# Optimization experiments

Measured on AMD Instinct MI355X. Metric: run time of the kernel, lower is better.

Reference implementation:

```python
import jax, jax.numpy as jnp
import numpy as np

B, T, D, H = 64, 512, 256, 512  # batch, seq_len, embed_dim, enc_units


def _lstm(x_tbd, U, xW, reverse):
    """Keras LSTM with activation='sigmoid' (all gates AND candidate/output use sigmoid).
    x_tbd: [T,B,D] (only for shape), xW: precomputed x@W+b [T,B,4H], U: [H,4H].
    Gate order in Keras kernels: i, f, c(g), o."""
    if reverse:
        xW = xW[::-1]
    b = xW.shape[1]
    h0 = jnp.zeros((b, U.shape[0]), xW.dtype)
    c0 = jnp.zeros((b, U.shape[0]), xW.dtype)

    def step(carry, xw):
        h, c = carry
        z = xw + h @ U  # [B,4H]
        i, f, g, o = jnp.split(z, 4, axis=-1)
        i = jax.nn.sigmoid(i)
        f = jax.nn.sigmoid(f)
        g = jax.nn.sigmoid(g)  # activation='sigmoid' (not tanh)
        o = jax.nn.sigmoid(o)
        c_new = f * c + i * g
        h_new = o * jax.nn.sigmoid(c_new)  # activation='sigmoid' (not tanh)
        return (h_new, c_new), h_new

    (h_last, c_last), hs = jax.lax.scan(step, (h0, c0), xW)
    if reverse:
        hs = hs[::-1]  # Bidirectional re-reverses backward outputs to align in time
    return hs, h_last, c_last


def setup_inputs() -> dict:
    key = jax.random.key(0)
    ks = jax.random.split(key, 6)
    s_in = 1.0 / np.sqrt(D)
    s_rec = 1.0 / np.sqrt(H)
    return {
        "x": jax.random.normal(ks[0], (B, T, D), jnp.float32),
        "hidden": jax.random.normal(ks[1], (2 * B, H), jnp.float32),  # unused by call()
        "Wf": jax.random.normal(ks[2], (D, 4 * H), jnp.float32) * s_in,
        "Uf": jax.random.normal(ks[3], (H, 4 * H), jnp.float32) * s_rec,
        "bf": jnp.zeros((4 * H,), jnp.float32),
        "Wb": jax.random.normal(ks[4], (D, 4 * H), jnp.float32) * s_in,
        "Ub": jax.random.normal(ks[5], (H, 4 * H), jnp.float32) * s_rec,
        "bb": jnp.zeros((4 * H,), jnp.float32),
    }


def reference(x, hidden, Wf, Uf, bf, Wb, Ub, bb):
    x_tbd = jnp.transpose(x, (1, 0, 2))  # [T,B,D]
    # Precompute input projections for all timesteps (hoisted out of the scan)
    xWf = jnp.einsum('tbd,dh->tbh', x_tbd, Wf) + bf
    xWb = jnp.einsum('tbd,dh->tbh', x_tbd, Wb) + bb
    hs_f, hF, cF = _lstm(x_tbd, Uf, xWf, reverse=False)
    hs_b, hB, cB = _lstm(x_tbd, Ub, xWb, reverse=True)
    out = 0.5 * (hs_f + hs_b)  # merge_mode='ave'
    out = jnp.transpose(out, (1, 0, 2))  # [B,T,H]
    return out, hF, cF, hB, cB
```

## Files before the change

### kernel.cpp

```cpp
#include <hip/hip_runtime.h>
#include <hip/hip_bf16.h>
#include <cstdint>
#include <cstddef>

#define BB 64
#define TT 512
#define DD 256
#define HH 512
#define G4 2048

typedef __bf16 bf16x8 __attribute__((ext_vector_type(8)));
typedef __bf16 bf16x4 __attribute__((ext_vector_type(4)));
typedef float  f32x4  __attribute__((ext_vector_type(4)));

__device__ __forceinline__ float sigf(float x) {
  return 1.0f / (1.0f + __expf(-x));
}

__global__ void cvt_x_kernel(const float* __restrict__ x, __bf16* __restrict__ xb) {
  int i = (blockIdx.x * 256 + threadIdx.x) * 4;
  float4 v = *(const float4*)(x + i);
  bf16x4 o;
  o[0] = (__bf16)v.x; o[1] = (__bf16)v.y; o[2] = (__bf16)v.z; o[3] = (__bf16)v.w;
  *(bf16x4*)(xb + i) = o;
}

__launch_bounds__(256, 1)
__global__ void lstm_kernel(const __bf16* __restrict__ xb,
                            const float* __restrict__ Wf, const float* __restrict__ Uf,
                            const float* __restrict__ bf_,
                            const float* __restrict__ Wb, const float* __restrict__ Ub,
                            const float* __restrict__ bb_,
                            __bf16* __restrict__ hbuf,
                            unsigned int* __restrict__ counters,
                            float* __restrict__ out,
                            __bf16* __restrict__ hsb) {
  const int bx  = blockIdx.x;
  const int dir = bx >> 5;
  const int s   = bx & 31;
  const float* Wd = dir ? Wb : Wf;
  const float* Ud = dir ? Ub : Uf;
  const float* bd = dir ? bb_ : bf_;
  unsigned int* cnt = counters + dir * 64;
  __bf16* hb = hbuf + (size_t)dir * 2 * BB * HH;

  const int tid  = threadIdx.x;
  const int mt   = tid >> 6;
  const int lane = tid & 63;
  const int j    = lane & 15;
  const int q    = lane >> 4;
  const int colg = s * 16 + j;

  bf16x8 wfrag[4][24];
#pragma unroll
  for (int g = 0; g < 4; ++g) {
    const int col = g * HH + colg;
#pragma unroll
    for (int kt = 0; kt < 24; ++kt) {
      bf16x8 v;
#pragma unroll
      for (int e = 0; e < 8; ++e) {
        const int k = kt * 32 + q * 8 + e;
        const float w = (k < DD) ? Wd[(size_t)k * G4 + col]
                                 : Ud[(size_t)(k - DD) * G4 + col];
        v[e] = (__bf16)w;
      }
      wfrag[g][kt] = v;
    }
  }
  float bg[4];
#pragma unroll
  for (int g = 0; g < 4; ++g) bg[g] = bd[g * HH + colg];

  float cst[4] = {0.f, 0.f, 0.f, 0.f};
  const size_t outTail = (size_t)BB * TT * HH;

  for (int tau = 0; tau < TT; ++tau) {
    const int t = dir ? (TT - 1 - tau) : tau;

    const __bf16* xrow = xb + ((size_t)(mt * 16 + j) * TT + t) * DD + q * 8;
    f32x4 acc[4];
#pragma unroll
    for (int g = 0; g < 4; ++g) acc[g] = (f32x4){bg[g], bg[g], bg[g], bg[g]};
#pragma unroll
    for (int kt = 0; kt < 8; ++kt) {
      bf16x8 a = *(const bf16x8*)(xrow + kt * 32);
#pragma unroll
      for (int g = 0; g < 4; ++g)
        acc[g] = __builtin_amdgcn_mfma_f32_16x16x32_bf16(a, wfrag[g][kt], acc[g], 0, 0, 0);
    }

    if (tau) {
      if (tid == 0) {
        const unsigned int target = 32u * (unsigned int)tau;
        while (__hip_atomic_load(cnt, __ATOMIC_ACQUIRE, __HIP_MEMORY_SCOPE_AGENT) < target)
          __builtin_amdgcn_s_sleep(2);
      }
      __syncthreads();
    }

    const __bf16* hrow = hb + (size_t)(tau & 1) * (BB * HH) + (size_t)(mt * 16 + j) * HH + q * 8;
#pragma unroll
    for (int kt = 0; kt < 16; ++kt) {
      bf16x8 a = *(const bf16x8*)(hrow + kt * 32);
#pragma unroll
      for (int g = 0; g < 4; ++g)
        acc[g] = __builtin_amdgcn_mfma_f32_16x16x32_bf16(a, wfrag[g][8 + kt], acc[g], 0, 0, 0);
    }

    __bf16* hnext = hb + (size_t)((tau + 1) & 1) * (BB * HH);
#pragma unroll
    for (int r = 0; r < 4; ++r) {
      const float zi = acc[0][r], zf = acc[1][r], zg = acc[2][r], zo = acc[3][r];
      const float gi = sigf(zi), gf = sigf(zf), gg = sigf(zg), go = sigf(zo);
      const float cn = gf * cst[r] + gi * gg;
      cst[r] = cn;
      const float hn = go * sigf(cn);
      const int orow = mt * 16 + q * 4 + r;
      hnext[(size_t)orow * HH + colg] = (__bf16)hn;
      if (dir == 0) {
        out[(size_t)orow * (TT * HH) + (size_t)t * HH + colg] = 0.5f * hn;
      } else {
        hsb[(size_t)t * (BB * HH) + (size_t)orow * HH + colg] = (__bf16)hn;
      }
      if (tau == TT - 1) {
        float* base = out + outTail + (size_t)dir * (2 * BB * HH);
        base[(size_t)orow * HH + colg] = hn;
        base[(size_t)BB * HH + (size_t)orow * HH + colg] = cn;
      }
    }

    __syncthreads();
    if (tid == 0)
      __hip_atomic_fetch_add(cnt, 1u, __ATOMIC_RELEASE, __HIP_MEMORY_SCOPE_AGENT);
  }
}

__global__ void combine_kernel(float* __restrict__ out, const __bf16* __restrict__ hsb) {
  const size_t i = ((size_t)blockIdx.x * 256 + threadIdx.x) * 4;
  const size_t b = i >> 18;
  const size_t t = (i >> 9) & 511;
  const size_t c = i & 511;
  bf16x4 hv = *(const bf16x4*)(hsb + t * (BB * HH) + b * HH + c);
  float4 v = *(float4*)(out + i);
  v.x += 0.5f * (float)hv[0];
  v.y += 0.5f * (float)hv[1];
  v.z += 0.5f * (float)hv[2];
  v.w += 0.5f * (float)hv[3];
  *(float4*)(out + i) = v;
}

extern "C" void kernel_launch(void* const* d_in, const int* in_sizes, int n_in,
                              void* d_out, int out_size, void* d_ws, size_t ws_size,
                              hipStream_t stream) {
  (void)in_sizes; (void)n_in; (void)out_size; (void)ws_size;
  const float* x   = (const float*)d_in[0];
  const float* Wf  = (const float*)d_in[2];
  const float* Uf  = (const float*)d_in[3];
  const float* bf_ = (const float*)d_in[4];
  const float* Wb  = (const float*)d_in[5];
  const float* Ub  = (const float*)d_in[6];
  const float* bb_ = (const float*)d_in[7];
  float* out = (float*)d_out;
  char* ws = (char*)d_ws;

  unsigned int* counters = (unsigned int*)ws;
  __bf16* hbuf = (__bf16*)(ws + 1024);
  __bf16* xb   = (__bf16*)(ws + (1 << 19));
  __bf16* hsb  = (__bf16*)(ws + (1 << 19) + (size_t)BB * TT * DD * 2);

  hipMemsetAsync(ws, 0, 1 << 19, stream);
  cvt_x_kernel<<<dim3((BB * TT * DD) / 1024), dim3(256), 0, stream>>>(x, xb);
  lstm_kernel<<<dim3(64), dim3(256), 0, stream>>>(xb, Wf, Uf, bf_, Wb, Ub, bb_,
                                                  hbuf, counters, out, hsb);
  combine_kernel<<<dim3((BB * TT * HH) / 1024), dim3(256), 0, stream>>>(out, hsb);
}
```

Measured before the change: 4.343 ms.

## Replace acquire/release grid barrier with relaxed coherent loads and per-thread polling

Every thread now polls the step counter itself with relaxed atomics instead of thread 0 spinning under acquire ordering followed by a __syncthreads. Hidden-state exchange uses agent-scope relaxed atomic loads and stores, so the data bypasses non-coherent caches without full cache invalidation or writeback fences. The recurrent h loads are double-buffered in registers, so loads for the next k-block are issued while the MFMAs for the current one run. Correctness now depends on compiler signal fences and the hardware coherence of the atomic accesses rather than on real acquire/release semantics, which risks stale reads.

```diff
diff --git a/kernel.cpp b/kernel.cpp
--- a/kernel.cpp
+++ b/kernel.cpp
@@ -12,9 +12,21 @@
 typedef __bf16 bf16x8 __attribute__((ext_vector_type(8)));
 typedef __bf16 bf16x4 __attribute__((ext_vector_type(4)));
 typedef float  f32x4  __attribute__((ext_vector_type(4)));
+typedef unsigned long long ull_t;
 
 __device__ __forceinline__ float sigf(float x) {
   return 1.0f / (1.0f + __expf(-x));
+}
+
+__device__ __forceinline__ ull_t coh_load_u64(const __bf16* p) {
+  return __hip_atomic_load(reinterpret_cast<const ull_t*>(p),
+                           __ATOMIC_RELAXED, __HIP_MEMORY_SCOPE_AGENT);
+}
+__device__ __forceinline__ void coh_store_bf16(__bf16* p, float v) {
+  union { __bf16 b; unsigned short u; } cv;
+  cv.b = (__bf16)v;
+  __hip_atomic_store(reinterpret_cast<unsigned short*>(p), cv.u,
+                     __ATOMIC_RELAXED, __HIP_MEMORY_SCOPE_AGENT);
 }
 
 __global__ void cvt_x_kernel(const float* __restrict__ x, __bf16* __restrict__ xb) {
@@ -78,6 +90,8 @@
   for (int tau = 0; tau < TT; ++tau) {
     const int t = dir ? (TT - 1 - tau) : tau;
 
+    const __bf16* hrow = hb + (size_t)(tau & 1) * (BB * HH) + (size_t)(mt * 16 + j) * HH + q * 8;
+
     const __bf16* xrow = xb + ((size_t)(mt * 16 + j) * TT + t) * DD + q * 8;
     f32x4 acc[4];
 #pragma unroll
@@ -91,21 +105,45 @@
     }
 
     if (tau) {
-      if (tid == 0) {
-        const unsigned int target = 32u * (unsigned int)tau;
-        while (__hip_atomic_load(cnt, __ATOMIC_ACQUIRE, __HIP_MEMORY_SCOPE_AGENT) < target)
-          __builtin_amdgcn_s_sleep(2);
-      }
-      __syncthreads();
-    }
-
-    const __bf16* hrow = hb + (size_t)(tau & 1) * (BB * HH) + (size_t)(mt * 16 + j) * HH + q * 8;
-#pragma unroll
-    for (int kt = 0; kt < 16; ++kt) {
-      bf16x8 a = *(const bf16x8*)(hrow + kt * 32);
-#pragma unroll
-      for (int g = 0; g < 4; ++g)
-        acc[g] = __builtin_amdgcn_mfma_f32_16x16x32_bf16(a, wfrag[g][8 + kt], acc[g], 0, 0, 0);
+      const unsigned int target = 32u * (unsigned int)tau;
+      while (__hip_atomic_load(cnt, __ATOMIC_RELAXED, __HIP_MEMORY_SCOPE_AGENT) < target) {
+        __builtin_amdgcn_s_sleep(1);
+      }
+      __atomic_signal_fence(__ATOMIC_ACQUIRE);
+      __builtin_amdgcn_sched_barrier(0);
+    }
+
+    {
+      ull_t pre[8];
+      ull_t nxt[8];
+#pragma unroll
+      for (int i = 0; i < 4; ++i) {
+        pre[2*i]   = coh_load_u64(hrow + i * 32);
+        pre[2*i+1] = coh_load_u64(hrow + i * 32 + 4);
+      }
+#pragma unroll
+      for (int kb = 0; kb < 4; ++kb) {
+        if (kb < 3) {
+#pragma unroll
+          for (int i = 0; i < 4; ++i) {
+            nxt[2*i]   = coh_load_u64(hrow + ((kb + 1) * 4 + i) * 32);
+            nxt[2*i+1] = coh_load_u64(hrow + ((kb + 1) * 4 + i) * 32 + 4);
+          }
+        }
+#pragma unroll
+        for (int i = 0; i < 4; ++i) {
+          union { ull_t q[2]; bf16x8 v; } uu;
+          uu.q[0] = pre[2*i]; uu.q[1] = pre[2*i+1];
+          const int kt = kb * 4 + i;
+#pragma unroll
+          for (int g = 0; g < 4; ++g)
+            acc[g] = __builtin_amdgcn_mfma_f32_16x16x32_bf16(uu.v, wfrag[g][8 + kt], acc[g], 0, 0, 0);
+        }
+        if (kb < 3) {
+#pragma unroll
+          for (int i = 0; i < 8; ++i) pre[i] = nxt[i];
+        }
+      }
     }
 
     __bf16* hnext = hb + (size_t)((tau + 1) & 1) * (BB * HH);
@@ -117,7 +155,7 @@
       cst[r] = cn;
       const float hn = go * sigf(cn);
       const int orow = mt * 16 + q * 4 + r;
-      hnext[(size_t)orow * HH + colg] = (__bf16)hn;
+      coh_store_bf16(&hnext[(size_t)orow * HH + colg], hn);
       if (dir == 0) {
         out[(size_t)orow * (TT * HH) + (size_t)t * HH + colg] = 0.5f * hn;
       } else {
@@ -130,9 +168,10 @@
       }
     }
 
+    __atomic_signal_fence(__ATOMIC_RELEASE);
     __syncthreads();
     if (tid == 0)
-      __hip_atomic_fetch_add(cnt, 1u, __ATOMIC_RELEASE, __HIP_MEMORY_SCOPE_AGENT);
+      __hip_atomic_fetch_add(cnt, 1u, __ATOMIC_RELAXED, __HIP_MEMORY_SCOPE_AGENT);
   }
 }
 
```

Measured after the change: 3.765 ms. -13.3%, faster.

## Replace counter barrier with epoch tags embedded in bf16 hidden-state bits

Applied to the files above, without the earlier changes.

Removes the per-step global atomic counter, the spin-wait and both __syncthreads. Each hidden-state value now carries a 2-bit epoch tag in the top bits of its bf16 word, which are always zero for outputs in (0,1). Consumer waves poll their own h fragments with coherent 64-bit loads until every tag matches the expected epoch, then strip the tags and issue the MFMAs. This cuts cross-block synchronisation latency on the serial recurrence. In exchange it adds repeated polling traffic, and correctness depends on h staying in (0,1) and on the 0xFF memset producing a tag that never matches.

```diff
diff --git a/kernel.cpp b/kernel.cpp
--- a/kernel.cpp
+++ b/kernel.cpp
@@ -12,9 +12,21 @@
 typedef __bf16 bf16x8 __attribute__((ext_vector_type(8)));
 typedef __bf16 bf16x4 __attribute__((ext_vector_type(4)));
 typedef float  f32x4  __attribute__((ext_vector_type(4)));
+typedef unsigned long long ull_t;
+
+#define TAGM 0xC000C000C000C000ULL
 
 __device__ __forceinline__ float sigf(float x) {
   return 1.0f / (1.0f + __expf(-x));
+}
+
+__device__ __forceinline__ ull_t coh_load_u64(const __bf16* p) {
+  return __hip_atomic_load(reinterpret_cast<const ull_t*>(p),
+                           __ATOMIC_RELAXED, __HIP_MEMORY_SCOPE_AGENT);
+}
+__device__ __forceinline__ void coh_store_u16(__bf16* p, unsigned short v) {
+  __hip_atomic_store(reinterpret_cast<unsigned short*>(p), v,
+                     __ATOMIC_RELAXED, __HIP_MEMORY_SCOPE_AGENT);
 }
 
 __global__ void cvt_x_kernel(const float* __restrict__ x, __bf16* __restrict__ xb) {
@@ -32,7 +44,6 @@
                             const float* __restrict__ Wb, const float* __restrict__ Ub,
                             const float* __restrict__ bb_,
                             __bf16* __restrict__ hbuf,
-                            unsigned int* __restrict__ counters,
                             float* __restrict__ out,
                             __bf16* __restrict__ hsb) {
   const int bx  = blockIdx.x;
@@ -41,7 +52,6 @@
   const float* Wd = dir ? Wb : Wf;
   const float* Ud = dir ? Ub : Uf;
   const float* bd = dir ? bb_ : bf_;
-  unsigned int* cnt = counters + dir * 64;
   __bf16* hb = hbuf + (size_t)dir * 2 * BB * HH;
 
   const int tid  = threadIdx.x;
@@ -91,23 +101,38 @@
     }
 
     if (tau) {
-      if (tid == 0) {
-        const unsigned int target = 32u * (unsigned int)tau;
-        while (__hip_atomic_load(cnt, __ATOMIC_ACQUIRE, __HIP_MEMORY_SCOPE_AGENT) < target)
-          __builtin_amdgcn_s_sleep(2);
-      }
-      __syncthreads();
-    }
-
-    const __bf16* hrow = hb + (size_t)(tau & 1) * (BB * HH) + (size_t)(mt * 16 + j) * HH + q * 8;
-#pragma unroll
-    for (int kt = 0; kt < 16; ++kt) {
-      bf16x8 a = *(const bf16x8*)(hrow + kt * 32);
-#pragma unroll
-      for (int g = 0; g < 4; ++g)
-        acc[g] = __builtin_amdgcn_mfma_f32_16x16x32_bf16(a, wfrag[g][8 + kt], acc[g], 0, 0, 0);
-    }
-
+      const __bf16* hrow = hb + (size_t)(tau & 1) * (BB * HH)
+                              + (size_t)(mt * 16 + j) * HH + q * 8;
+      const ull_t epat = (ull_t)(1u + ((unsigned)(tau >> 1) & 1u)) * 0x4000400040004000ULL;
+#pragma unroll
+      for (int kb = 0; kb < 4; ++kb) {
+        ull_t d[8];
+        int ok;
+        do {
+#pragma unroll
+          for (int i = 0; i < 4; ++i) {
+            d[2*i]   = coh_load_u64(hrow + (kb * 4 + i) * 32);
+            d[2*i+1] = coh_load_u64(hrow + (kb * 4 + i) * 32 + 4);
+          }
+          ok = 1;
+#pragma unroll
+          for (int i = 0; i < 8; ++i) ok &= ((d[i] & TAGM) == epat);
+        } while (!__all(ok));
+#pragma unroll
+        for (int i = 0; i < 4; ++i) {
+          union { ull_t u[2]; bf16x8 v; } uu;
+          uu.u[0] = d[2*i]   & ~TAGM;
+          uu.u[1] = d[2*i+1] & ~TAGM;
+          const int kt = kb * 4 + i;
+#pragma unroll
+          for (int g = 0; g < 4; ++g)
+            acc[g] = __builtin_amdgcn_mfma_f32_16x16x32_bf16(uu.v, wfrag[g][8 + kt], acc[g], 0, 0, 0);
+        }
+      }
+    }
+
+    const unsigned short ptag =
+        (unsigned short)((1u + ((unsigned)((tau + 1) >> 1) & 1u)) << 14);
     __bf16* hnext = hb + (size_t)((tau + 1) & 1) * (BB * HH);
 #pragma unroll
     for (int r = 0; r < 4; ++r) {
@@ -117,7 +142,10 @@
       cst[r] = cn;
       const float hn = go * sigf(cn);
       const int orow = mt * 16 + q * 4 + r;
-      hnext[(size_t)orow * HH + colg] = (__bf16)hn;
+      union { __bf16 b; unsigned short u; } cv;
+      cv.b = (__bf16)hn;
+      coh_store_u16(&hnext[(size_t)orow * HH + colg],
+                    (unsigned short)(cv.u | ptag));
       if (dir == 0) {
         out[(size_t)orow * (TT * HH) + (size_t)t * HH + colg] = 0.5f * hn;
       } else {
@@ -129,10 +157,6 @@
         base[(size_t)BB * HH + (size_t)orow * HH + colg] = cn;
       }
     }
-
-    __syncthreads();
-    if (tid == 0)
-      __hip_atomic_fetch_add(cnt, 1u, __ATOMIC_RELEASE, __HIP_MEMORY_SCOPE_AGENT);
   }
 }
 
@@ -164,14 +188,13 @@
   float* out = (float*)d_out;
   char* ws = (char*)d_ws;
 
-  unsigned int* counters = (unsigned int*)ws;
   __bf16* hbuf = (__bf16*)(ws + 1024);
   __bf16* xb   = (__bf16*)(ws + (1 << 19));
   __bf16* hsb  = (__bf16*)(ws + (1 << 19) + (size_t)BB * TT * DD * 2);
 
-  hipMemsetAsync(ws, 0, 1 << 19, stream);
+  hipMemsetAsync(ws, 0xFF, 1 << 19, stream);
   cvt_x_kernel<<<dim3((BB * TT * DD) / 1024), dim3(256), 0, stream>>>(x, xb);
   lstm_kernel<<<dim3(64), dim3(256), 0, stream>>>(xb, Wf, Uf, bf_, Wb, Ub, bb_,
-                                                  hbuf, counters, out, hsb);
+                                                  hbuf, out, hsb);
   combine_kernel<<<dim3((BB * TT * HH) / 1024), dim3(256), 0, stream>>>(out, hsb);
 }
```

New measurement: 3.758 ms. -13.5%, faster.
